# Performance work log

Hardware: AMD Instinct MI355X
Metric: run time of the kernel (lower is better)

Reference implementation:

```python
import jax, jax.numpy as jnp
import numpy as np

NEG = -100.0  # MaxPlusSemiring.zero
V, E = 50000, 300
B, L = 64, 512
P, M = 200, 7          # num patterns, pattern length
D = M * 2 * P          # diag rows
H, C = 100, 2          # mlp hidden, classes


def setup_inputs() -> dict:
    key = jax.random.key(0)
    ks = jax.random.split(key, 12)
    diags = jax.random.normal(ks[1], (D, E), jnp.float32)
    diags = diags / jnp.linalg.norm(diags, axis=1, keepdims=True)  # normalize() in __init__
    return {
        "docs": jax.random.randint(ks[0], (B, L), 0, V),
        "embeddings": jax.random.normal(ks[2], (V, E), jnp.float32),
        "diags": diags,
        "bias": jax.random.normal(ks[3], (D,), jnp.float32),
        "epsilon": jax.random.normal(ks[4], (P, M - 1), jnp.float32),
        "w1": jax.random.normal(ks[5], (P, H), jnp.float32) * 0.05,
        "b1": jnp.zeros((H,), jnp.float32),
        "w2": jax.random.normal(ks[6], (H, H), jnp.float32) * 0.05,
        "b2": jnp.zeros((H,), jnp.float32),
        "w3": jax.random.normal(ks[7], (H, C), jnp.float32) * 0.05,
        "b3": jnp.zeros((C,), jnp.float32),
    }


def _sopa(docs, embeddings, diags, bias, epsilon, w1, b1, w2, b2, w3, b3):
    # transition scores: semiring.from_float = identity for MaxPlus
    emb = embeddings[docs]                                   # [B,L,E]
    ts = jnp.einsum('ble,de->bld', emb, diags) + bias        # [B,L,D]
    T = ts.reshape(B, L, P, 2, M)                            # [B,L,P,diag,M]

    h0 = jnp.full((B, P, M), NEG, ts.dtype).at[:, :, 0].set(0.0)  # one at start state
    s0 = jnp.full((B, P), NEG, ts.dtype)
    zero_pad = jnp.full((B, P, 1), NEG, ts.dtype)            # semiring.zero
    restart = jnp.zeros((B, P, 1), ts.dtype)                 # semiring.one
    eps = epsilon[None]                                      # eps_scale=0 -> identity; [1,P,M-1]

    def step(carry, x):  # x: [B,P,2,M]
        h, s = carry
        after_eps = jnp.maximum(h, jnp.concatenate([zero_pad, h[:, :, :-1] + eps], axis=2))
        main = jnp.concatenate([restart, after_eps[:, :, :-1] + x[:, :, 1, :-1]], axis=2)
        self_loop = after_eps + x[:, :, 0, :]                # self_loop_scale = 0 (identity)
        h_new = jnp.maximum(main, self_loop)
        s_new = jnp.maximum(s, h_new[:, :, -1])              # end state = M-1 for all patterns
        return (h_new, s_new), None

    (_, scores), _ = jax.lax.scan(step, (h0, s0), jnp.moveaxis(T, 1, 0))

    hidden = jax.nn.relu(scores @ w1 + b1)
    hidden = jax.nn.relu(hidden @ w2 + b2)
    return jax.nn.log_softmax(hidden @ w3 + b3, axis=-1)


def reference(docs, embeddings, diags, bias, epsilon, w1, b1, w2, b2, w3, b3):
    return _sopa(docs, embeddings, diags, bias, epsilon, w1, b1, w2, b2, w3, b3)
```

## Files before the change

### kernel.cpp

```cpp
#include <hip/hip_runtime.h>
#include <stdint.h>

#define NEG (-100.0f)

#define NE 300
#define NB 64
#define NL 512
#define NP 200
#define ND 2800
#define NH 100

#define KP 320
#define UNITS 40
#define ROWB 640

#define PT 8
#define DT 112
#define NTILE 25
#define LC 32
#define NCHUNK 16
#define SCW 36

#define LDS_A   (LC*ROWB)
#define LDS_SC  (DT*SCW*4)
#define LDS_TOTAL (2*LDS_A + 2*LDS_SC)

using f32x4  = __attribute__((ext_vector_type(4))) float;
using bf16x8 = __attribute__((ext_vector_type(8))) __bf16;

static __device__ __forceinline__ uint16_t f2bf(float f) {
    union { float f; uint32_t u; } v; v.f = f;
    return (uint16_t)((v.u + 0x7FFFu + ((v.u >> 16) & 1u)) >> 16);
}

static __device__ __forceinline__ void pin(bf16x8& x) {
    asm volatile("" : "+v"(x));
}

static __device__ __forceinline__ float dpp_shr1(float x) {
    int r = __builtin_amdgcn_update_dpp(0, __float_as_int(x), 0x111, 0xF, 0xF, true);
    return __int_as_float(r);
}

__global__ void prep_kernel(const int* __restrict__ docs,
                            const float* __restrict__ emb,
                            const float* __restrict__ diags,
                            const float* __restrict__ bias,
                            uint16_t* __restrict__ A_ws,
                            uint16_t* __restrict__ B_ws)
{
    int tid = blockIdx.x * blockDim.x + threadIdx.x;
    const int totalA = NB * NL * UNITS;
    const int total  = totalA + ND * UNITS;
    if (tid >= total) return;
    const float* src; uint16_t* dst; float extra; int r, j;
    if (tid < totalA) {
        r = tid / UNITS; j = tid - r * UNITS;
        src = emb + (size_t)docs[r] * NE;
        dst = A_ws + (size_t)r * KP;
        extra = 1.0f;
    } else {
        int t2 = tid - totalA;
        r = t2 / UNITS; j = t2 - r * UNITS;
        src = diags + (size_t)r * NE;
        dst = B_ws + (size_t)r * KP;
        extra = bias[r];
    }
    int jp = j ^ (r & 7);
    union { uint16_t h[8]; uint4 v; } u;
    if (j < 37) {
        float4 f0 = *reinterpret_cast<const float4*>(src + j * 8);
        float4 f1 = *reinterpret_cast<const float4*>(src + j * 8 + 4);
        u.h[0] = f2bf(f0.x); u.h[1] = f2bf(f0.y);
        u.h[2] = f2bf(f0.z); u.h[3] = f2bf(f0.w);
        u.h[4] = f2bf(f1.x); u.h[5] = f2bf(f1.y);
        u.h[6] = f2bf(f1.z); u.h[7] = f2bf(f1.w);
    } else if (j == 37) {
        float4 f0 = *reinterpret_cast<const float4*>(src + 296);
        u.h[0] = f2bf(f0.x); u.h[1] = f2bf(f0.y);
        u.h[2] = f2bf(f0.z); u.h[3] = f2bf(f0.w);
        u.h[4] = f2bf(extra); u.h[5] = 0; u.h[6] = 0; u.h[7] = 0;
    } else {
        u.v = uint4{0, 0, 0, 0};
    }
    *reinterpret_cast<uint4*>(dst + (size_t)jp * 8) = u.v;
}

template<int NFR>
static __device__ __forceinline__ void mfma_body(const char* __restrict__ Ab,
    const bf16x8 (&breg)[4][10], float* __restrict__ scw,
    int abase, int aswz, int cb, int rlo, int kq, int wr)
{
    f32x4 acc[NFR];
#pragma unroll
    for (int f = 0; f < NFR; ++f) acc[f] = f32x4{0.f, 0.f, 0.f, 0.f};
#pragma unroll
    for (int kk = 0; kk < KP / 32; ++kk) {
        int ab = abase + kk * 64 + kq * 16;
        bf16x8 av = *reinterpret_cast<const bf16x8*>(Ab + (ab ^ aswz));
#pragma unroll
        for (int f = 0; f < NFR; ++f)
            acc[f] = __builtin_amdgcn_mfma_f32_16x16x32_bf16(av, breg[f][kk], acc[f], 0, 0, 0);
    }
    const int crow = wr * 16 + kq * 4;
#pragma unroll
    for (int f = 0; f < NFR; ++f) {
        int col = (cb + f) * 16 + rlo;
        *reinterpret_cast<f32x4*>(scw + col * SCW + crow) = acc[f];
    }
}

static __device__ __forceinline__ void scan_chunk(const float* __restrict__ sc,
        float& h, float& s, float eps_r, bool is_m0, int i0, int i1)
{
    f32x4 xav[8], xbv[8];
#pragma unroll
    for (int i = 0; i < 8; ++i)
        xav[i] = *reinterpret_cast<const f32x4*>(sc + i0 * SCW + i * 4);
#pragma unroll
    for (int i = 0; i < 8; ++i)
        xbv[i] = *reinterpret_cast<const f32x4*>(sc + i1 * SCW + i * 4);
#pragma unroll
    for (int l = 0; l < LC; ++l) {
        float xa = xav[l >> 2][l & 3];
        float xb = xbv[l >> 2][l & 3];
        float hm1  = dpp_shr1(h);
        float t    = is_m0 ? NEG : (hm1 + eps_r);
        float ae   = fmaxf(h, t);
        float aem1 = dpp_shr1(ae);
        float mn   = is_m0 ? 0.0f : (aem1 + xb);
        h = fmaxf(mn, ae + xa);
        s = fmaxf(s, h);
    }
}

__global__ __launch_bounds__(512, 2)
void sopa_kernel(const uint16_t* __restrict__ A_ws,
                 const uint16_t* __restrict__ B_ws,
                 const float* __restrict__ epsilon,
                 float* __restrict__ scores_g)
{
    extern __shared__ char smem[];

    const int blk = blockIdx.x;
    const int bb  = blk / NTILE;
    const int pt  = blk - bb * NTILE;
    const int d0  = pt * DT;
    const int p0  = pt * PT;

    const int tid  = threadIdx.x;
    const int wave = tid >> 6;
    const int lane = tid & 63;

    const int rlo = lane & 15;
    const int kq  = lane >> 4;
    const int wr  = wave & 1;
    const int wc  = wave >> 1;
    const int cb  = wc * 4;
    const int nfr = (wc == 0) ? 4 : 3;
    const int arow  = wr * 16 + rlo;
    const int abase = arow * ROWB;
    const int aswz  = (arow & 7) << 4;

    bf16x8 breg[4][10];
    if (wave < 4) {
        const uint16_t* Bg = B_ws + (size_t)d0 * KP;
#pragma unroll
        for (int f = 0; f < 4; ++f) {
#pragma unroll
            for (int kk = 0; kk < 10; ++kk) {
                if (f < nfr) {
                    int col = (cb + f) * 16 + rlo;
                    int jp  = (kk * 4 + kq) ^ (col & 7);
                    breg[f][kk] = *reinterpret_cast<const bf16x8*>(
                        Bg + (size_t)col * KP + jp * 8);
                } else {
                    breg[f][kk] = bf16x8{0,0,0,0,0,0,0,0};
                }
                pin(breg[f][kk]);
            }
        }
    }

    {
        const uint4* a4 = (const uint4*)(A_ws + (size_t)(bb * NL) * KP);
        uint4* ad = (uint4*)smem;
        for (int u = tid; u < LDS_A / 16; u += 512) ad[u] = a4[u];
    }
    __syncthreads();

    const int  pp = lane >> 3;
    const int  mm = lane & 7;
    const bool is_m0 = (mm == 0);
    float eps_r = 0.0f;
    if (mm >= 1 && mm <= 6) eps_r = epsilon[(p0 + pp) * 6 + (mm - 1)];
    const int i0 = pp * 14 + mm;
    const int i1 = pp * 14 + 7 + (mm ? mm - 1 : 0);
    float h = is_m0 ? 0.0f : NEG;
    float s = NEG;

    for (int c = 0; c < NCHUNK; ++c) {
        if (wave < 4) {
            const char* Ab  = smem + (c & 1) * LDS_A;
            float*      scw = (float*)(smem + 2 * LDS_A + (c & 1) * LDS_SC);
            if (wc == 0) mfma_body<4>(Ab, breg, scw, abase, aswz, cb, rlo, kq, wr);
            else         mfma_body<3>(Ab, breg, scw, abase, aswz, cb, rlo, kq, wr);
        } else if (wave == 4) {
            if (c > 0) {
                const float* scr = (const float*)(smem + 2 * LDS_A + ((c - 1) & 1) * LDS_SC);
                scan_chunk(scr, h, s, eps_r, is_m0, i0, i1);
            }
        } else {
            if (c + 1 < NCHUNK) {
                const uint4* s4 = (const uint4*)(A_ws + (size_t)(bb * NL + (c + 1) * LC) * KP);
                uint4* d4 = (uint4*)(smem + ((c + 1) & 1) * LDS_A);
                const int sl = tid - 320;
                uint4 r0 = s4[sl];
                uint4 r1 = s4[sl + 192];
                uint4 r2 = s4[sl + 384];
                uint4 r3 = s4[sl + 576];
                uint4 r4 = s4[sl + 768];
                uint4 r5 = s4[sl + 960];
                uint4 r6 = uint4{0, 0, 0, 0};
                const bool t6 = sl < (LDS_A / 16 - 1152);
                if (t6) r6 = s4[sl + 1152];
                d4[sl]       = r0;
                d4[sl + 192] = r1;
                d4[sl + 384] = r2;
                d4[sl + 576] = r3;
                d4[sl + 768] = r4;
                d4[sl + 960] = r5;
                if (t6) d4[sl + 1152] = r6;
            }
        }
        __syncthreads();
    }

    if (wave == 4) {
        const float* scr = (const float*)(smem + 2 * LDS_A + ((NCHUNK - 1) & 1) * LDS_SC);
        scan_chunk(scr, h, s, eps_r, is_m0, i0, i1);
        if (mm == 6) scores_g[bb * NP + p0 + pp] = s;
    }
}

__global__ void mlp_kernel(const float* __restrict__ scores_g,
                           const float* __restrict__ w1, const float* __restrict__ b1,
                           const float* __restrict__ w2, const float* __restrict__ b2,
                           const float* __restrict__ w3, const float* __restrict__ b3,
                           float* __restrict__ out)
{
    __shared__ float sc[NP];
    __shared__ float h1[NH];
    __shared__ float h2[NH];
    int b = blockIdx.x, t = threadIdx.x;
    for (int i = t; i < NP; i += blockDim.x) sc[i] = scores_g[b * NP + i];
    __syncthreads();
    if (t < NH) {
        float acc = b1[t];
#pragma unroll 8
        for (int k = 0; k < NP; ++k) acc += sc[k] * w1[k * NH + t];
        h1[t] = fmaxf(acc, 0.0f);
    }
    __syncthreads();
    if (t < NH) {
        float acc = b2[t];
#pragma unroll 8
        for (int k = 0; k < NH; ++k) acc += h1[k] * w2[k * NH + t];
        h2[t] = fmaxf(acc, 0.0f);
    }
    __syncthreads();
    if (t < 64) {
        float l0 = 0.0f, l1 = 0.0f;
        for (int k = t; k < NH; k += 64) {
            float hv = h2[k];
            l0 += hv * w3[k * 2];
            l1 += hv * w3[k * 2 + 1];
        }
#pragma unroll
        for (int off = 32; off > 0; off >>= 1) {
            l0 += __shfl_down(l0, off);
            l1 += __shfl_down(l1, off);
        }
        if (t == 0) {
            l0 += b3[0]; l1 += b3[1];
            float mx  = fmaxf(l0, l1);
            float lse = mx + logf(expf(l0 - mx) + expf(l1 - mx));
            out[b * 2 + 0] = l0 - lse;
            out[b * 2 + 1] = l1 - lse;
        }
    }
}

extern "C" void kernel_launch(void* const* d_in, const int* in_sizes, int n_in,
                              void* d_out, int out_size, void* d_ws, size_t ws_size,
                              hipStream_t stream)
{
    const int*   docs  = (const int*)  d_in[0];
    const float* emb   = (const float*)d_in[1];
    const float* diags = (const float*)d_in[2];
    const float* bias  = (const float*)d_in[3];
    const float* eps   = (const float*)d_in[4];
    const float* w1 = (const float*)d_in[5];
    const float* b1 = (const float*)d_in[6];
    const float* w2 = (const float*)d_in[7];
    const float* b2 = (const float*)d_in[8];
    const float* w3 = (const float*)d_in[9];
    const float* b3 = (const float*)d_in[10];
    float* out = (float*)d_out;

    char* ws = (char*)d_ws;
    uint16_t* A_ws     = (uint16_t*)ws;
    uint16_t* B_ws     = (uint16_t*)(ws + 20971520);
    float*    scores_g = (float*)   (ws + 20971520 + 1792000);

    {
        int totalUnits = (NB * NL + ND) * UNITS;
        int blocks = (totalUnits + 255) / 256;
        prep_kernel<<<blocks, 256, 0, stream>>>(docs, emb, diags, bias, A_ws, B_ws);
    }

    (void)hipFuncSetAttribute(reinterpret_cast<const void*>(sopa_kernel),
                              hipFuncAttributeMaxDynamicSharedMemorySize, LDS_TOTAL);
    sopa_kernel<<<NB * NTILE, 512, LDS_TOTAL, stream>>>(A_ws, B_ws, eps, scores_g);

    mlp_kernel<<<NB, 128, 0, stream>>>(scores_g, w1, b1, w2, b2, w3, b3, out);
}
```

Before: 308.8 us.

## Triple-buffer A tiles with async global-to-LDS loads and split scan across two waves

Replaces the register-staged copy of document embedding tiles with direct global_load_lds transfers into a three-deep LDS ring, prefetching two chunks ahead and using raw s_barrier with explicit waitcnts instead of __syncthreads. The scan work is split across two waves (4 patterns each) to shorten the serial recurrence per chunk. B fragments are always loaded (padded workspace), so breg is no longer zero-filled conditionally. This is meant to hide global memory latency behind MFMA and scan work, at the cost of extra LDS and more delicate synchronization.

```diff
diff --git a/kernel.cpp b/kernel.cpp
--- a/kernel.cpp
+++ b/kernel.cpp
@@ -8,6 +8,7 @@
 #define NL 512
 #define NP 200
 #define ND 2800
+#define NDP 2816
 #define NH 100
 
 #define KP 320
@@ -23,10 +24,22 @@
 
 #define LDS_A   (LC*ROWB)
 #define LDS_SC  (DT*SCW*4)
-#define LDS_TOTAL (2*LDS_A + 2*LDS_SC)
+#define LDS_TOTAL (3*LDS_A + 2*LDS_SC)
 
 using f32x4  = __attribute__((ext_vector_type(4))) float;
 using bf16x8 = __attribute__((ext_vector_type(8))) __bf16;
+
+#define SBAR()       asm volatile("s_barrier" ::: "memory")
+#define WAIT_LGKM0() do { asm volatile("s_waitcnt lgkmcnt(0)" ::: "memory"); \
+                          __builtin_amdgcn_sched_barrier(0); } while (0)
+#define WAIT_VM(N)   do { asm volatile("s_waitcnt vmcnt(" #N ")" ::: "memory"); \
+                          __builtin_amdgcn_sched_barrier(0); } while (0)
+
+static __device__ __forceinline__ void gload16(const void* g, void* l) {
+    __builtin_amdgcn_global_load_lds(
+        (const __attribute__((address_space(1))) void*)g,
+        (__attribute__((address_space(3))) void*)l, 16, 0, 0);
+}
 
 static __device__ __forceinline__ uint16_t f2bf(float f) {
     union { float f; uint32_t u; } v; v.f = f;
@@ -88,7 +101,7 @@
 
 template<int NFR>
 static __device__ __forceinline__ void mfma_body(const char* __restrict__ Ab,
-    const bf16x8 (&breg)[4][10], float* __restrict__ scw,
+    const bf16x8 (&breg)[40], float* __restrict__ scw,
     int abase, int aswz, int cb, int rlo, int kq, int wr)
 {
     f32x4 acc[NFR];
@@ -100,7 +113,7 @@
         bf16x8 av = *reinterpret_cast<const bf16x8*>(Ab + (ab ^ aswz));
 #pragma unroll
         for (int f = 0; f < NFR; ++f)
-            acc[f] = __builtin_amdgcn_mfma_f32_16x16x32_bf16(av, breg[f][kk], acc[f], 0, 0, 0);
+            acc[f] = __builtin_amdgcn_mfma_f32_16x16x32_bf16(av, breg[f * 10 + kk], acc[f], 0, 0, 0);
     }
     const int crow = wr * 16 + kq * 4;
 #pragma unroll
@@ -155,91 +168,86 @@
     const int rlo = lane & 15;
     const int kq  = lane >> 4;
     const int wr  = wave & 1;
-    const int wc  = wave >> 1;
+    const int wc  = (wave >> 1) & 1;
     const int cb  = wc * 4;
-    const int nfr = (wc == 0) ? 4 : 3;
     const int arow  = wr * 16 + rlo;
     const int abase = arow * ROWB;
     const int aswz  = (arow & 7) << 4;
 
-    bf16x8 breg[4][10];
+    bf16x8 breg[40];
     if (wave < 4) {
         const uint16_t* Bg = B_ws + (size_t)d0 * KP;
 #pragma unroll
         for (int f = 0; f < 4; ++f) {
 #pragma unroll
             for (int kk = 0; kk < 10; ++kk) {
-                if (f < nfr) {
-                    int col = (cb + f) * 16 + rlo;
-                    int jp  = (kk * 4 + kq) ^ (col & 7);
-                    breg[f][kk] = *reinterpret_cast<const bf16x8*>(
-                        Bg + (size_t)col * KP + jp * 8);
-                } else {
-                    breg[f][kk] = bf16x8{0,0,0,0,0,0,0,0};
-                }
-                pin(breg[f][kk]);
+                const int col = (cb + f) * 16 + rlo;
+                const int jp  = (kk * 4 + kq) ^ (col & 7);
+                breg[f * 10 + kk] = *reinterpret_cast<const bf16x8*>(
+                    Bg + (size_t)col * KP + jp * 8);
+                pin(breg[f * 10 + kk]);
             }
         }
     }
 
-    {
-        const uint4* a4 = (const uint4*)(A_ws + (size_t)(bb * NL) * KP);
-        uint4* ad = (uint4*)smem;
-        for (int u = tid; u < LDS_A / 16; u += 512) ad[u] = a4[u];
-    }
-    __syncthreads();
-
-    const int  pp = lane >> 3;
+    const int  q  = lane >> 3;
     const int  mm = lane & 7;
+    const int  pl = ((wave == 5) ? 4 : 0) + (q & 3);
     const bool is_m0 = (mm == 0);
     float eps_r = 0.0f;
-    if (mm >= 1 && mm <= 6) eps_r = epsilon[(p0 + pp) * 6 + (mm - 1)];
-    const int i0 = pp * 14 + mm;
-    const int i1 = pp * 14 + 7 + (mm ? mm - 1 : 0);
+    if (mm >= 1 && mm <= 6) eps_r = epsilon[(p0 + pl) * 6 + (mm - 1)];
+    const int i0 = pl * 14 + mm;
+    const int i1 = pl * 14 + 7 + (mm ? mm - 1 : 0);
     float h = is_m0 ? 0.0f : NEG;
     float s = NEG;
 
+    const int   wv    = wave & 1;
+    const char* a_src = (const char*)(A_ws + (size_t)bb * NL * KP) + wv * 10240 + lane * 16;
+
+    if (wave >= 6) {
+#pragma unroll
+        for (int i = 0; i < 10; ++i)
+            gload16(a_src + i * 1024, smem + wv * 10240 + i * 1024);
+#pragma unroll
+        for (int i = 0; i < 10; ++i)
+            gload16(a_src + LC * ROWB + i * 1024, smem + LDS_A + wv * 10240 + i * 1024);
+        WAIT_VM(10);
+    }
+    SBAR();
+
     for (int c = 0; c < NCHUNK; ++c) {
         if (wave < 4) {
-            const char* Ab  = smem + (c & 1) * LDS_A;
-            float*      scw = (float*)(smem + 2 * LDS_A + (c & 1) * LDS_SC);
+            const char* Ab  = smem + (c % 3) * LDS_A;
+            float*      scw = (float*)(smem + 3 * LDS_A + (c & 1) * LDS_SC);
             if (wc == 0) mfma_body<4>(Ab, breg, scw, abase, aswz, cb, rlo, kq, wr);
             else         mfma_body<3>(Ab, breg, scw, abase, aswz, cb, rlo, kq, wr);
-        } else if (wave == 4) {
+            WAIT_LGKM0();
+            SBAR();
+        } else if (wave < 6) {
             if (c > 0) {
-                const float* scr = (const float*)(smem + 2 * LDS_A + ((c - 1) & 1) * LDS_SC);
+                const float* scr = (const float*)(smem + 3 * LDS_A + ((c - 1) & 1) * LDS_SC);
                 scan_chunk(scr, h, s, eps_r, is_m0, i0, i1);
             }
+            SBAR();
         } else {
-            if (c + 1 < NCHUNK) {
-                const uint4* s4 = (const uint4*)(A_ws + (size_t)(bb * NL + (c + 1) * LC) * KP);
-                uint4* d4 = (uint4*)(smem + ((c + 1) & 1) * LDS_A);
-                const int sl = tid - 320;
-                uint4 r0 = s4[sl];
-                uint4 r1 = s4[sl + 192];
-                uint4 r2 = s4[sl + 384];
-                uint4 r3 = s4[sl + 576];
-                uint4 r4 = s4[sl + 768];
-                uint4 r5 = s4[sl + 960];
-                uint4 r6 = uint4{0, 0, 0, 0};
-                const bool t6 = sl < (LDS_A / 16 - 1152);
-                if (t6) r6 = s4[sl + 1152];
-                d4[sl]       = r0;
-                d4[sl + 192] = r1;
-                d4[sl + 384] = r2;
-                d4[sl + 576] = r3;
-                d4[sl + 768] = r4;
-                d4[sl + 960] = r5;
-                if (t6) d4[sl + 1152] = r6;
+            if (c + 2 < NCHUNK) {
+                const char* src = a_src + (size_t)(c + 2) * LC * ROWB;
+                char*       lb  = smem + ((c + 2) % 3) * LDS_A + wv * 10240;
+#pragma unroll
+                for (int i = 0; i < 10; ++i)
+                    gload16(src + i * 1024, lb + i * 1024);
+                WAIT_VM(10);
+            } else {
+                WAIT_VM(0);
             }
-        }
-        __syncthreads();
-    }
-
-    if (wave == 4) {
-        const float* scr = (const float*)(smem + 2 * LDS_A + ((NCHUNK - 1) & 1) * LDS_SC);
+            SBAR();
+        }
+    }
+
+    if (wave == 4 || wave == 5) {
+        const float* scr = (const float*)(smem + 3 * LDS_A + ((NCHUNK - 1) & 1) * LDS_SC);
         scan_chunk(scr, h, s, eps_r, is_m0, i0, i1);
-        if (mm == 6) scores_g[bb * NP + p0 + pp] = s;
+        if (q < 4 && mm == 6) scores_g[bb * NP + p0 + pl] = s;
     }
 }
 
@@ -311,7 +319,7 @@
     char* ws = (char*)d_ws;
     uint16_t* A_ws     = (uint16_t*)ws;
     uint16_t* B_ws     = (uint16_t*)(ws + 20971520);
-    float*    scores_g = (float*)   (ws + 20971520 + 1792000);
+    float*    scores_g = (float*)   (ws + 20971520 + 1802240);
 
     {
         int totalUnits = (NB * NL + ND) * UNITS;
```

Result: no change. 303.7 us (-1.6%).
